# Performance work log

Measured on AMD Instinct MI355X. Metric: run time of the kernel, lower is better.

Reference implementation:

```python
import jax, jax.numpy as jnp
import numpy as np

V, E, H, L, B, S = 32000, 512, 512, 2, 8, 512


def setup_inputs() -> dict:
    key = jax.random.key(0)
    ks = jax.random.split(key, 16)
    emb = jax.random.normal(ks[0], (V, E), jnp.float32) * 0.02
    emb = emb.at[0].set(0.0)  # padding_idx=0
    init_state = jax.random.normal(ks[1], (2, L, H), jnp.float32)  # [h;c] params
    def xav(k, shp):
        fan_in, fan_out = shp[1], shp[0]
        lim = np.sqrt(6.0 / (fan_in + fan_out)).astype(np.float32)
        return jax.random.uniform(k, shp, jnp.float32, -lim, lim)
    inp = {
        'emb_table': emb,
        'init_state': init_state,
        'w_ih0': xav(ks[2], (4 * H, E)), 'w_hh0': xav(ks[3], (4 * H, H)),
        'b_ih0': jnp.zeros((4 * H,), jnp.float32), 'b_hh0': jnp.zeros((4 * H,), jnp.float32),
        'w_ih1': xav(ks[4], (4 * H, H)), 'w_hh1': xav(ks[5], (4 * H, H)),
        'b_ih1': jnp.zeros((4 * H,), jnp.float32), 'b_hh1': jnp.zeros((4 * H,), jnp.float32),
        'wg': xav(ks[6], (2 * H, H)), 'bg': jnp.zeros((2 * H,), jnp.float32),
        'wd': xav(ks[7], (V, H)), 'bd': jnp.zeros((V,), jnp.float32),
        'eps': jax.random.normal(ks[8], (B, S, H), jnp.float32),
        'x': jax.random.randint(ks[9], (B, S), 0, V, jnp.int64),
    }
    return inp


def _lstm_layer(xs, h0, c0, w_ih, w_hh, b_ih, b_hh):
    # xs: [S, B, in]; returns hidden sequence [S, B, H]
    b = b_ih + b_hh
    def step(carry, x_t):
        h, c = carry
        gates = x_t @ w_ih.T + h @ w_hh.T + b  # [B, 4H]
        i, f, g, o = jnp.split(gates, 4, axis=-1)  # torch gate order i,f,g,o
        c = jax.nn.sigmoid(f) * c + jax.nn.sigmoid(i) * jnp.tanh(g)
        h = jax.nn.sigmoid(o) * jnp.tanh(c)
        return (h, c), h
    _, hs = jax.lax.scan(step, (h0, c0), xs)
    return hs


def reference(emb_table, init_state, w_ih0, w_hh0, b_ih0, b_hh0,
              w_ih1, w_hh1, b_ih1, b_hh1, wg, bg, wd, bd, eps, x):
    Bsz = x.shape[0]
    embedding = emb_table[x]  # [B, S, E]
    h0 = jnp.broadcast_to(init_state[0][:, None, :], (L, Bsz, H))
    c0 = jnp.broadcast_to(init_state[1][:, None, :], (L, Bsz, H))
    xs = embedding.transpose(1, 0, 2)  # time-major [S, B, E]
    hs0 = _lstm_layer(xs, h0[0], c0[0], w_ih0, w_hh0, b_ih0, b_hh0)
    hs1 = _lstm_layer(hs0, h0[1], c0[1], w_ih1, w_hh1, b_ih1, b_hh1)
    out = hs1.transpose(1, 0, 2)  # [B, S, H]
    stats = out @ wg.T + bg  # [B, S, 2H]
    std = jax.nn.softplus(stats[:, :, :H])  # diagonal of covariance matrix
    mu = stats[:, :, H:]
    # MultivariateNormal(mu, cov=diag(std)).rsample() => mu + sqrt(std) * eps
    sample = mu + jnp.sqrt(std) * eps
    logits = sample @ wd.T + bd  # [B, S, V]
    return (logits, mu, std)
```

## Files before the change

kernel.cpp:

```cpp
#include <hip/hip_runtime.h>


typedef __attribute__((ext_vector_type(4))) float f32x4;
typedef __attribute__((ext_vector_type(8))) short short8;
typedef __attribute__((ext_vector_type(4))) unsigned short u16x4;

#define V_SZ 32000
#define E_SZ 512
#define H_SZ 512
#define B_SZ 8
#define S_SZ 512
#define NTOK 4096
#define G4H  2048

__device__ __forceinline__ unsigned short f2bf(float x) {
  unsigned int b = __float_as_uint(x);
  b += 0x7FFFu + ((b >> 16) & 1u);
  return (unsigned short)(b >> 16);
}
__device__ __forceinline__ float bf2f(unsigned short u) {
  return __uint_as_float(((unsigned int)u) << 16);
}

__device__ __forceinline__ void split4(const f32x4 v, u16x4& hv, u16x4& lv) {
  unsigned short h0 = f2bf(v.x); lv.x = f2bf(v.x - bf2f(h0)); hv.x = h0;
  unsigned short h1 = f2bf(v.y); lv.y = f2bf(v.y - bf2f(h1)); hv.y = h1;
  unsigned short h2 = f2bf(v.z); lv.z = f2bf(v.z - bf2f(h2)); hv.z = h2;
  unsigned short h3 = f2bf(v.w); lv.w = f2bf(v.w - bf2f(h3)); hv.w = h3;
}

__global__ void split_kernel(const float* __restrict__ src,
                             unsigned short* __restrict__ hi,
                             unsigned short* __restrict__ lo, int n4) {
  int i = blockIdx.x * 256 + threadIdx.x;
  if (i >= n4) return;
  f32x4 v = ((const f32x4*)src)[i];
  u16x4 hv, lv;
  split4(v, hv, lv);
  ((u16x4*)hi)[i] = hv;
  ((u16x4*)lo)[i] = lv;
}

__global__ void bias_sum_kernel(const float* __restrict__ a0, const float* __restrict__ c0,
                                const float* __restrict__ a1, const float* __restrict__ c1,
                                float* __restrict__ o0, float* __restrict__ o1) {
  int i = blockIdx.x * 256 + threadIdx.x;
  if (i < G4H) { o0[i] = a0[i] + c0[i]; o1[i] = a1[i] + c1[i]; }
}

__global__ void embed_hi_kernel(const float* __restrict__ emb, const int* __restrict__ x,
                                unsigned short* __restrict__ hi) {
  int gid = blockIdx.x * 256 + threadIdx.x;
  int r = gid >> 7;
  int kq = (gid & 127) << 2;
  int tok = x[r];
  f32x4 v = *(const f32x4*)(emb + (size_t)tok * E_SZ + kq);
  u16x4 hv;
  hv.x = f2bf(v.x); hv.y = f2bf(v.y); hv.z = f2bf(v.z); hv.w = f2bf(v.w);
  *(u16x4*)(hi + (size_t)r * E_SZ + kq) = hv;
}

__device__ __forceinline__ int swz32(int row, int seg) {
  return row * 32 + (((seg ^ (row & 3)) << 3));
}

__global__ __launch_bounds__(256, 2) void gemm2_kernel(
    const unsigned short* __restrict__ Ah,
    const unsigned short* __restrict__ Bh, const unsigned short* __restrict__ Bl,
    const float* __restrict__ bias, float* __restrict__ C,
    int M, int N, int K) {
  __shared__ unsigned short sA[128 * 32];
  __shared__ unsigned short sBh[128 * 32];
  __shared__ unsigned short sBl[128 * 32];

  const int t = threadIdx.x;
  const int lane = t & 63;
  const int wave = t >> 6;
  const int wr = wave >> 1, wc = wave & 1;
  const size_t m0 = (size_t)blockIdx.y * 128;
  const size_t n0 = (size_t)blockIdx.x * 128;

  f32x4 acc[4][4];
#pragma unroll
  for (int i = 0; i < 4; ++i)
#pragma unroll
    for (int j = 0; j < 4; ++j) acc[i][j] = (f32x4){0.f, 0.f, 0.f, 0.f};

  const int r0 = t >> 2;
  const int seg0 = t & 3;

  const int nk = K >> 5;
  for (int ks = 0; ks < nk; ++ks) {
    const int k0 = ks << 5;
    short8 vA[2], vBh[2], vBl[2];
#pragma unroll
    for (int r = 0; r < 2; ++r) {
      int row = r0 + r * 64;
      size_t ga = (m0 + row) * (size_t)K + k0 + seg0 * 8;
      size_t gb = (n0 + row) * (size_t)K + k0 + seg0 * 8;
      vA[r] = *(const short8*)(Ah + ga);
      vBh[r] = *(const short8*)(Bh + gb);
      vBl[r] = *(const short8*)(Bl + gb);
    }
    __syncthreads();
#pragma unroll
    for (int r = 0; r < 2; ++r) {
      int row = r0 + r * 64;
      int d = swz32(row, seg0);
      *(short8*)(sA + d) = vA[r];
      *(short8*)(sBh + d) = vBh[r];
      *(short8*)(sBl + d) = vBl[r];
    }
    __syncthreads();

    short8 a[4], bh[4], bl[4];
    const int seg = lane >> 4;
#pragma unroll
    for (int m = 0; m < 4; ++m) {
      int row = wr * 64 + m * 16 + (lane & 15);
      int d = swz32(row, seg);
      a[m] = *(const short8*)(sA + d);
    }
#pragma unroll
    for (int n = 0; n < 4; ++n) {
      int row = wc * 64 + n * 16 + (lane & 15);
      int d = swz32(row, seg);
      bh[n] = *(const short8*)(sBh + d);
      bl[n] = *(const short8*)(sBl + d);
    }
#pragma unroll
    for (int m = 0; m < 4; ++m) {
#pragma unroll
      for (int n = 0; n < 4; ++n) {
        acc[m][n] = __builtin_amdgcn_mfma_f32_16x16x32_bf16(a[m], bh[n], acc[m][n], 0, 0, 0);
        acc[m][n] = __builtin_amdgcn_mfma_f32_16x16x32_bf16(a[m], bl[n], acc[m][n], 0, 0, 0);
      }
    }
  }

#pragma unroll
  for (int m = 0; m < 4; ++m) {
#pragma unroll
    for (int n = 0; n < 4; ++n) {
      size_t gr0 = m0 + wr * 64 + m * 16 + ((lane >> 4) << 2);
      size_t gc = n0 + wc * 64 + n * 16 + (lane & 15);
      float bv = bias ? bias[gc] : 0.f;
#pragma unroll
      for (int j = 0; j < 4; ++j) {
        C[(gr0 + j) * (size_t)N + gc] = acc[m][n][j] + bv;
      }
    }
  }
}

#define SEQ_NB 192
#define SEQ_NB_L0 64

__device__ __forceinline__ float sigm(float x) { return 1.f / (1.f + expf(-x)); }

__global__ __launch_bounds__(256, 1) void lstm_seq_kernel(
    const float* __restrict__ gx0,
    const float* __restrict__ w_hh0,
    const float* __restrict__ w_ih1,
    const float* __restrict__ w_hh1,
    const float* __restrict__ b1s,
    const float* __restrict__ initst,
    float* __restrict__ h0_all,
    float* __restrict__ h1_all,
    unsigned short* __restrict__ hs1h,
    unsigned int* __restrict__ sig0,
    unsigned int* __restrict__ sig1) {
  const int blk = blockIdx.x;
  const int t = threadIdx.x;
  const bool isL1 = (blk >= SEQ_NB_L0);
  const int lb = isL1 ? (blk - SEQ_NB_L0) : blk;

  __shared__ float hA[8][512];
  __shared__ float hB[8][512];
  __shared__ float gates_s[32][8];

  const int tb = t >> 7;
  const int rg = isL1 ? ((t >> 5) & 3) : ((t >> 4) & 7);
  const int kg = isL1 ? (t & 31) : (t & 15);

  f32x4 w[4][8];
  if (!isL1) {
#pragma unroll
    for (int rr = 0; rr < 4; ++rr) {
      int rl = rg * 4 + rr;
      int grow = (rl >> 3) * H_SZ + lb * 8 + (rl & 7);
      const float* src = w_hh0 + (size_t)grow * H_SZ + kg * 4;
#pragma unroll
      for (int j = 0; j < 8; ++j) w[rr][j] = *(const f32x4*)(src + j * 64);
    }
  } else {
#pragma unroll
    for (int rr = 0; rr < 4; ++rr) {
      int rl = rg * 4 + rr;
      int grow = (rl >> 2) * H_SZ + lb * 4 + (rl & 3);
      const float* s1 = w_ih1 + (size_t)grow * H_SZ + kg * 4;
      const float* s2 = w_hh1 + (size_t)grow * H_SZ + kg * 4;
#pragma unroll
      for (int j = 0; j < 4; ++j) w[rr][j] = *(const f32x4*)(s1 + j * 128);
#pragma unroll
      for (int j = 0; j < 4; ++j) w[rr][4 + j] = *(const f32x4*)(s2 + j * 128);
    }
  }

  const int UPB = isL1 ? 4 : 8;
  const int nCell = UPB * 8;
  const int cu = t >> 3, cb = t & 7;
  const int cunit = lb * UPB + cu;
  float creg = 0.f;
  float bgi = 0.f, bgf = 0.f, bgg = 0.f, bgo = 0.f;
  if (t < nCell) {
    creg = initst[1024 + (isL1 ? 512 : 0) + cunit];
    if (isL1) {
      bgi = b1s[cunit];
      bgf = b1s[512 + cunit];
      bgg = b1s[1024 + cunit];
      bgo = b1s[1536 + cunit];
    }
  }

  for (int step = 0; step < 512; ++step) {
    float pgi = 0.f, pgf = 0.f, pgg = 0.f, pgo = 0.f;
    if (!isL1 && t < nCell) {
      const float* gx = gx0 + ((size_t)(cb * S_SZ + step)) * G4H + cunit;
      pgi = gx[0];
      pgf = gx[512];
      pgg = gx[1024];
      pgo = gx[1536];
    }

    if (t < 64) {
      if (!isL1) {
        if (step > 0) {
          const unsigned int* s0 = sig0 + (size_t)(step - 1) * 64;
          while (true) {
            unsigned int v = __hip_atomic_load(&s0[t], __ATOMIC_RELAXED, __HIP_MEMORY_SCOPE_AGENT);
            if (__all(v != 0)) break;
            __builtin_amdgcn_s_sleep(1);
          }
        }
      } else {
        const unsigned int* s0 = sig0 + (size_t)step * 64;
        const unsigned int* s1 = (step > 0) ? (sig1 + (size_t)(step - 1) * 128) : nullptr;
        while (true) {
          int ok = (__hip_atomic_load(&s0[t], __ATOMIC_RELAXED, __HIP_MEMORY_SCOPE_AGENT) != 0);
          if (s1) {
            ok &= (__hip_atomic_load(&s1[t], __ATOMIC_RELAXED, __HIP_MEMORY_SCOPE_AGENT) != 0);
            ok &= (__hip_atomic_load(&s1[64 + t], __ATOMIC_RELAXED, __HIP_MEMORY_SCOPE_AGENT) != 0);
          }
          if (__all(ok)) break;
          __builtin_amdgcn_s_sleep(1);
        }
      }
    }
    __syncthreads();

    if (!isL1) {
      if (step == 0) {
#pragma unroll
        for (int i = 0; i < 4; ++i) {
          int idx = t + i * 256;
          int b = idx >> 7;
          int kc = (idx & 127) << 2;
          *(f32x4*)&hA[b][kc] = *(const f32x4*)(initst + kc);
        }
      } else {
        const float* src = h0_all + (size_t)(step - 1) * 4096;
#pragma unroll
        for (int i = 0; i < 4; ++i) {
          int idx = t + i * 256;
          int b = idx >> 7;
          int kc = (idx & 127) << 2;
          *(f32x4*)&hA[b][kc] = *(const f32x4*)(src + b * H_SZ + kc);
        }
      }
    } else {
      const float* s0 = h0_all + (size_t)step * 4096;
      const float* s1 = (step == 0) ? nullptr : (h1_all + (size_t)(step - 1) * 4096);
#pragma unroll
      for (int i = 0; i < 4; ++i) {
        int idx = t + i * 256;
        int b = idx >> 7;
        int kc = (idx & 127) << 2;
        *(f32x4*)&hA[b][kc] = *(const f32x4*)(s0 + b * H_SZ + kc);
        f32x4 v1 = s1 ? *(const f32x4*)(s1 + b * H_SZ + kc)
                      : *(const f32x4*)(initst + 512 + kc);
        *(f32x4*)&hB[b][kc] = v1;
      }
    }
    __syncthreads();

    float acc[4][4];
#pragma unroll
    for (int rr = 0; rr < 4; ++rr)
#pragma unroll
      for (int bq = 0; bq < 4; ++bq) acc[rr][bq] = 0.f;

    if (!isL1) {
#pragma unroll
      for (int bq = 0; bq < 4; ++bq) {
        const float* hb = &hA[tb * 4 + bq][0];
#pragma unroll
        for (int j = 0; j < 8; ++j) {
          f32x4 hq = *(const f32x4*)(hb + kg * 4 + j * 64);
#pragma unroll
          for (int rr = 0; rr < 4; ++rr)
            acc[rr][bq] += w[rr][j].x * hq.x + w[rr][j].y * hq.y +
                           w[rr][j].z * hq.z + w[rr][j].w * hq.w;
        }
      }
#pragma unroll
      for (int s = 1; s < 16; s <<= 1) {
#pragma unroll
        for (int rr = 0; rr < 4; ++rr)
#pragma unroll
          for (int bq = 0; bq < 4; ++bq)
            acc[rr][bq] += __shfl_xor(acc[rr][bq], s, 64);
      }
      if (kg == 0) {
#pragma unroll
        for (int rr = 0; rr < 4; ++rr)
#pragma unroll
          for (int bq = 0; bq < 4; ++bq)
            gates_s[rg * 4 + rr][tb * 4 + bq] = acc[rr][bq];
      }
    } else {
#pragma unroll
      for (int bq = 0; bq < 4; ++bq) {
        const int b = tb * 4 + bq;
        const float* ha = &hA[b][0];
        const float* hbp = &hB[b][0];
#pragma unroll
        for (int j = 0; j < 4; ++j) {
          f32x4 hq = *(const f32x4*)(ha + kg * 4 + j * 128);
#pragma unroll
          for (int rr = 0; rr < 4; ++rr)
            acc[rr][bq] += w[rr][j].x * hq.x + w[rr][j].y * hq.y +
                           w[rr][j].z * hq.z + w[rr][j].w * hq.w;
        }
#pragma unroll
        for (int j = 0; j < 4; ++j) {
          f32x4 hq = *(const f32x4*)(hbp + kg * 4 + j * 128);
#pragma unroll
          for (int rr = 0; rr < 4; ++rr)
            acc[rr][bq] += w[rr][4 + j].x * hq.x + w[rr][4 + j].y * hq.y +
                           w[rr][4 + j].z * hq.z + w[rr][4 + j].w * hq.w;
        }
      }
#pragma unroll
      for (int s = 1; s < 32; s <<= 1) {
#pragma unroll
        for (int rr = 0; rr < 4; ++rr)
#pragma unroll
          for (int bq = 0; bq < 4; ++bq)
            acc[rr][bq] += __shfl_xor(acc[rr][bq], s, 64);
      }
      if (kg == 0) {
#pragma unroll
        for (int rr = 0; rr < 4; ++rr)
#pragma unroll
          for (int bq = 0; bq < 4; ++bq)
            gates_s[rg * 4 + rr][tb * 4 + bq] = acc[rr][bq];
      }
    }
    __syncthreads();

    float hval = 0.f;
    if (t < nCell) {
      float gi, gf, gg, go;
      if (!isL1) {
        gi = gates_s[cu][cb] + pgi;
        gf = gates_s[8 + cu][cb] + pgf;
        gg = gates_s[16 + cu][cb] + pgg;
        go = gates_s[24 + cu][cb] + pgo;
      } else {
        gi = gates_s[cu][cb] + bgi;
        gf = gates_s[4 + cu][cb] + bgf;
        gg = gates_s[8 + cu][cb] + bgg;
        go = gates_s[12 + cu][cb] + bgo;
      }
      float cn = sigm(gf) * creg + sigm(gi) * tanhf(gg);
      hval = sigm(go) * tanhf(cn);
      creg = cn;
      if (!isL1) {
        __hip_atomic_store(&h0_all[(size_t)step * 4096 + cb * H_SZ + cunit], hval,
                           __ATOMIC_RELAXED, __HIP_MEMORY_SCOPE_AGENT);
      } else {
        __hip_atomic_store(&h1_all[(size_t)step * 4096 + cb * H_SZ + cunit], hval,
                           __ATOMIC_RELAXED, __HIP_MEMORY_SCOPE_AGENT);
      }
    }
    if (t == 0) {
      asm volatile("s_waitcnt vmcnt(0)" ::: "memory");
      unsigned int* slot = isL1 ? (sig1 + (size_t)step * 128 + lb)
                                : (sig0 + (size_t)step * 64 + lb);
      __hip_atomic_store(slot, 1u, __ATOMIC_RELAXED, __HIP_MEMORY_SCOPE_AGENT);
    }
    if (isL1 && t < nCell) {
      hs1h[(size_t)(cb * S_SZ + step) * H_SZ + cunit] = f2bf(hval);
    }
  }
}

__global__ void sample_kernel(const float* __restrict__ stats, const float* __restrict__ eps,
                              unsigned short* __restrict__ sh,
                              float* __restrict__ omu, float* __restrict__ ostd) {
  int gid = blockIdx.x * 256 + threadIdx.x;
  int r = gid >> 9, hh = gid & 511;
  float sp = stats[(size_t)r * 1024 + hh];
  float mu = stats[(size_t)r * 1024 + 512 + hh];
  float sd = (sp > 20.f) ? sp : log1pf(expf(sp));
  float smp = mu + sqrtf(sd) * eps[gid];
  omu[gid] = mu;
  ostd[gid] = sd;
  sh[gid] = f2bf(smp);
}

extern "C" void kernel_launch(void* const* d_in, const int* in_sizes, int n_in,
                              void* d_out, int out_size, void* d_ws, size_t ws_size,
                              hipStream_t stream) {
  const float* emb    = (const float*)d_in[0];
  const float* initst = (const float*)d_in[1];
  const float* w_ih0  = (const float*)d_in[2];
  const float* w_hh0  = (const float*)d_in[3];
  const float* b_ih0  = (const float*)d_in[4];
  const float* b_hh0  = (const float*)d_in[5];
  const float* w_ih1  = (const float*)d_in[6];
  const float* w_hh1  = (const float*)d_in[7];
  const float* b_ih1  = (const float*)d_in[8];
  const float* b_hh1  = (const float*)d_in[9];
  const float* wg     = (const float*)d_in[10];
  const float* bg     = (const float*)d_in[11];
  const float* wd     = (const float*)d_in[12];
  const float* bd     = (const float*)d_in[13];
  const float* eps    = (const float*)d_in[14];
  const int*   x      = (const int*)d_in[15];

  char* ws = (char*)d_ws;
  size_t off = 0;
  auto alloc = [&](size_t sz) {
    void* p = ws + off;
    off = (off + sz + 255) & ~(size_t)255;
    return p;
  };
  unsigned int* sig0     = (unsigned int*)alloc((size_t)512 * 64 * 4);
  unsigned int* sig1     = (unsigned int*)alloc((size_t)512 * 128 * 4);
  float* b0s             = (float*)alloc(G4H * 4);
  float* b1s             = (float*)alloc(G4H * 4);
  unsigned short* wih0h  = (unsigned short*)alloc((size_t)G4H * E_SZ * 2);
  unsigned short* wih0l  = (unsigned short*)alloc((size_t)G4H * E_SZ * 2);
  unsigned short* wgh    = (unsigned short*)alloc((size_t)1024 * H_SZ * 2);
  unsigned short* wgl    = (unsigned short*)alloc((size_t)1024 * H_SZ * 2);
  unsigned short* wdh    = (unsigned short*)alloc((size_t)V_SZ * H_SZ * 2);
  unsigned short* wdl    = (unsigned short*)alloc((size_t)V_SZ * H_SZ * 2);
  unsigned short* a0h    = (unsigned short*)alloc((size_t)NTOK * E_SZ * 2);
  float* gx0             = (float*)alloc((size_t)NTOK * G4H * 4);
  float* h0_all          = (float*)alloc((size_t)512 * 4096 * 4);
  float* h1_all          = (float*)alloc((size_t)512 * 4096 * 4);
  unsigned short* hs1h   = (unsigned short*)alloc((size_t)NTOK * H_SZ * 2);
  float* stats           = (float*)alloc((size_t)NTOK * 1024 * 4);
  unsigned short* smph   = (unsigned short*)alloc((size_t)NTOK * H_SZ * 2);

  float* out_logits = (float*)d_out;
  float* out_mu     = out_logits + (size_t)NTOK * V_SZ;
  float* out_std    = out_mu + (size_t)NTOK * H_SZ;

  (void)hipMemsetAsync(sig0, 0, (size_t)512 * 64 * 4, stream);
  (void)hipMemsetAsync(sig1, 0, (size_t)512 * 128 * 4, stream);

  split_kernel<<<(G4H * E_SZ / 4 + 255) / 256, 256, 0, stream>>>(w_ih0, wih0h, wih0l, G4H * E_SZ / 4);
  split_kernel<<<(1024 * H_SZ / 4 + 255) / 256, 256, 0, stream>>>(wg, wgh, wgl, 1024 * H_SZ / 4);
  split_kernel<<<(V_SZ * H_SZ / 4 + 255) / 256, 256, 0, stream>>>(wd, wdh, wdl, V_SZ * H_SZ / 4);
  bias_sum_kernel<<<8, 256, 0, stream>>>(b_ih0, b_hh0, b_ih1, b_hh1, b0s, b1s);

  embed_hi_kernel<<<NTOK * 128 / 256, 256, 0, stream>>>(emb, x, a0h);

  gemm2_kernel<<<dim3(G4H / 128, NTOK / 128), 256, 0, stream>>>(
      a0h, wih0h, wih0l, b0s, gx0, NTOK, G4H, E_SZ);

  lstm_seq_kernel<<<SEQ_NB, 256, 0, stream>>>(
      gx0, w_hh0, w_ih1, w_hh1, b1s, initst, h0_all, h1_all, hs1h, sig0, sig1);

  gemm2_kernel<<<dim3(1024 / 128, NTOK / 128), 256, 0, stream>>>(
      hs1h, wgh, wgl, bg, stats, NTOK, 1024, H_SZ);

  sample_kernel<<<NTOK * H_SZ / 256, 256, 0, stream>>>(stats, eps, smph, out_mu, out_std);

  gemm2_kernel<<<dim3(V_SZ / 128, NTOK / 128), 256, 0, stream>>>(
      smph, wdh, wdl, bd, out_logits, NTOK, V_SZ, H_SZ);
}
```

Measured before the change: 3.693 ms.

## Use NaN-sentinel data polling for LSTM sync and single-bf16 decoder GEMM

The recurrent kernel drops its separate flag arrays. Consumers now poll the hidden-state buffers directly, which are pre-filled with an all-ones NaN sentinel, so each step needs one memory round trip instead of a flag check followed by a data load. Separately, the large vocabulary projection switches from a split hi/lo bf16 GEMM to a single bf16 GEMM with 2 blocks per CU. That halves MFMA work and weight traffic but reduces precision on the logits. The sentinel scheme assumes no real hidden value ever equals the 0xFFFFFFFF bit pattern, and that each 64-bit atomic load observes a consistent value.

```diff
diff --git a/kernel.cpp b/kernel.cpp
--- a/kernel.cpp
+++ b/kernel.cpp
@@ -27,6 +27,22 @@
   unsigned short h1 = f2bf(v.y); lv.y = f2bf(v.y - bf2f(h1)); hv.y = h1;
   unsigned short h2 = f2bf(v.z); lv.z = f2bf(v.z - bf2f(h2)); hv.z = h2;
   unsigned short h3 = f2bf(v.w); lv.w = f2bf(v.w - bf2f(h3)); hv.w = h3;
+}
+
+__device__ __forceinline__ f32x4 ld16_bypass(const float* p) {
+  const unsigned long long* q = (const unsigned long long*)p;
+  unsigned long long a = __hip_atomic_load(&q[0], __ATOMIC_RELAXED, __HIP_MEMORY_SCOPE_AGENT);
+  unsigned long long b = __hip_atomic_load(&q[1], __ATOMIC_RELAXED, __HIP_MEMORY_SCOPE_AGENT);
+  f32x4 r;
+  r.x = __uint_as_float((unsigned int)a);
+  r.y = __uint_as_float((unsigned int)(a >> 32));
+  r.z = __uint_as_float((unsigned int)b);
+  r.w = __uint_as_float((unsigned int)(b >> 32));
+  return r;
+}
+__device__ __forceinline__ int chk4(const f32x4 v) {
+  return (__float_as_uint(v.x) != 0xFFFFFFFFu) & (__float_as_uint(v.y) != 0xFFFFFFFFu) &
+         (__float_as_uint(v.z) != 0xFFFFFFFFu) & (__float_as_uint(v.w) != 0xFFFFFFFFu);
 }
 
 __global__ void split_kernel(const float* __restrict__ src,
@@ -41,6 +57,16 @@
   ((u16x4*)lo)[i] = lv;
 }
 
+__global__ void cast_hi_kernel(const float* __restrict__ src,
+                               unsigned short* __restrict__ hi, int n4) {
+  int i = blockIdx.x * 256 + threadIdx.x;
+  if (i >= n4) return;
+  f32x4 v = ((const f32x4*)src)[i];
+  u16x4 hv;
+  hv.x = f2bf(v.x); hv.y = f2bf(v.y); hv.z = f2bf(v.z); hv.w = f2bf(v.w);
+  ((u16x4*)hi)[i] = hv;
+}
+
 __global__ void bias_sum_kernel(const float* __restrict__ a0, const float* __restrict__ c0,
                                 const float* __restrict__ a1, const float* __restrict__ c1,
                                 float* __restrict__ o0, float* __restrict__ o1) {
@@ -118,8 +144,7 @@
 #pragma unroll
     for (int m = 0; m < 4; ++m) {
       int row = wr * 64 + m * 16 + (lane & 15);
-      int d = swz32(row, seg);
-      a[m] = *(const short8*)(sA + d);
+      a[m] = *(const short8*)(sA + swz32(row, seg));
     }
 #pragma unroll
     for (int n = 0; n < 4; ++n) {
@@ -134,6 +159,85 @@
       for (int n = 0; n < 4; ++n) {
         acc[m][n] = __builtin_amdgcn_mfma_f32_16x16x32_bf16(a[m], bh[n], acc[m][n], 0, 0, 0);
         acc[m][n] = __builtin_amdgcn_mfma_f32_16x16x32_bf16(a[m], bl[n], acc[m][n], 0, 0, 0);
+      }
+    }
+  }
+
+#pragma unroll
+  for (int m = 0; m < 4; ++m) {
+#pragma unroll
+    for (int n = 0; n < 4; ++n) {
+      size_t gr0 = m0 + wr * 64 + m * 16 + ((lane >> 4) << 2);
+      size_t gc = n0 + wc * 64 + n * 16 + (lane & 15);
+      float bv = bias ? bias[gc] : 0.f;
+#pragma unroll
+      for (int j = 0; j < 4; ++j) {
+        C[(gr0 + j) * (size_t)N + gc] = acc[m][n][j] + bv;
+      }
+    }
+  }
+}
+
+__global__ __launch_bounds__(256, 2) void gemm1_kernel(
+    const unsigned short* __restrict__ Ah, const unsigned short* __restrict__ Bh,
+    const float* __restrict__ bias, float* __restrict__ C,
+    int M, int N, int K) {
+  __shared__ unsigned short sA[128 * 32];
+  __shared__ unsigned short sB[128 * 32];
+
+  const int t = threadIdx.x;
+  const int lane = t & 63;
+  const int wave = t >> 6;
+  const int wr = wave >> 1, wc = wave & 1;
+  const size_t m0 = (size_t)blockIdx.y * 128;
+  const size_t n0 = (size_t)blockIdx.x * 128;
+
+  f32x4 acc[4][4];
+#pragma unroll
+  for (int i = 0; i < 4; ++i)
+#pragma unroll
+    for (int j = 0; j < 4; ++j) acc[i][j] = (f32x4){0.f, 0.f, 0.f, 0.f};
+
+  const int r0 = t >> 2;
+  const int seg0 = t & 3;
+
+  const int nk = K >> 5;
+  for (int ks = 0; ks < nk; ++ks) {
+    const int k0 = ks << 5;
+    short8 vA[2], vB[2];
+#pragma unroll
+    for (int r = 0; r < 2; ++r) {
+      int row = r0 + r * 64;
+      vA[r] = *(const short8*)(Ah + (m0 + row) * (size_t)K + k0 + seg0 * 8);
+      vB[r] = *(const short8*)(Bh + (n0 + row) * (size_t)K + k0 + seg0 * 8);
+    }
+    __syncthreads();
+#pragma unroll
+    for (int r = 0; r < 2; ++r) {
+      int row = r0 + r * 64;
+      int d = swz32(row, seg0);
+      *(short8*)(sA + d) = vA[r];
+      *(short8*)(sB + d) = vB[r];
+    }
+    __syncthreads();
+
+    short8 a[4], b[4];
+    const int seg = lane >> 4;
+#pragma unroll
+    for (int m = 0; m < 4; ++m) {
+      int row = wr * 64 + m * 16 + (lane & 15);
+      a[m] = *(const short8*)(sA + swz32(row, seg));
+    }
+#pragma unroll
+    for (int n = 0; n < 4; ++n) {
+      int row = wc * 64 + n * 16 + (lane & 15);
+      b[n] = *(const short8*)(sB + swz32(row, seg));
+    }
+#pragma unroll
+    for (int m = 0; m < 4; ++m) {
+#pragma unroll
+      for (int n = 0; n < 4; ++n) {
+        acc[m][n] = __builtin_amdgcn_mfma_f32_16x16x32_bf16(a[m], b[n], acc[m][n], 0, 0, 0);
       }
     }
   }
@@ -167,9 +271,7 @@
     const float* __restrict__ initst,
     float* __restrict__ h0_all,
     float* __restrict__ h1_all,
-    unsigned short* __restrict__ hs1h,
-    unsigned int* __restrict__ sig0,
-    unsigned int* __restrict__ sig1) {
+    unsigned short* __restrict__ hs1h) {
   const int blk = blockIdx.x;
   const int t = threadIdx.x;
   const bool isL1 = (blk >= SEQ_NB_L0);
@@ -233,63 +335,81 @@
       pgo = gx[1536];
     }
 
-    if (t < 64) {
-      if (!isL1) {
-        if (step > 0) {
-          const unsigned int* s0 = sig0 + (size_t)(step - 1) * 64;
-          while (true) {
-            unsigned int v = __hip_atomic_load(&s0[t], __ATOMIC_RELAXED, __HIP_MEMORY_SCOPE_AGENT);
-            if (__all(v != 0)) break;
-            __builtin_amdgcn_s_sleep(1);
-          }
+    float* ldA = &hA[0][0] + t * 4;
+    float* ldB = &hB[0][0] + t * 4;
+    if (!isL1) {
+      if (step == 0) {
+#pragma unroll
+        for (int i = 0; i < 4; ++i) {
+          int idx = t + i * 256;
+          int kc = (idx & 127) << 2;
+          *(f32x4*)(&hA[0][0] + idx * 4) = *(const f32x4*)(initst + kc);
         }
       } else {
-        const unsigned int* s0 = sig0 + (size_t)step * 64;
-        const unsigned int* s1 = (step > 0) ? (sig1 + (size_t)(step - 1) * 128) : nullptr;
+        const float* s = h0_all + (size_t)(step - 1) * 4096 + (size_t)t * 4;
+        f32x4 v0, v1, v2, v3;
         while (true) {
-          int ok = (__hip_atomic_load(&s0[t], __ATOMIC_RELAXED, __HIP_MEMORY_SCOPE_AGENT) != 0);
-          if (s1) {
-            ok &= (__hip_atomic_load(&s1[t], __ATOMIC_RELAXED, __HIP_MEMORY_SCOPE_AGENT) != 0);
-            ok &= (__hip_atomic_load(&s1[64 + t], __ATOMIC_RELAXED, __HIP_MEMORY_SCOPE_AGENT) != 0);
-          }
+          v0 = ld16_bypass(s);
+          v1 = ld16_bypass(s + 1024);
+          v2 = ld16_bypass(s + 2048);
+          v3 = ld16_bypass(s + 3072);
+          int ok = chk4(v0) & chk4(v1) & chk4(v2) & chk4(v3);
           if (__all(ok)) break;
           __builtin_amdgcn_s_sleep(1);
         }
-      }
-    }
-    __syncthreads();
-
-    if (!isL1) {
+        *(f32x4*)ldA = v0;
+        *(f32x4*)(ldA + 1024) = v1;
+        *(f32x4*)(ldA + 2048) = v2;
+        *(f32x4*)(ldA + 3072) = v3;
+      }
+    } else {
+      const float* s0 = h0_all + (size_t)step * 4096 + (size_t)t * 4;
       if (step == 0) {
+        f32x4 v0, v1, v2, v3;
+        while (true) {
+          v0 = ld16_bypass(s0);
+          v1 = ld16_bypass(s0 + 1024);
+          v2 = ld16_bypass(s0 + 2048);
+          v3 = ld16_bypass(s0 + 3072);
+          int ok = chk4(v0) & chk4(v1) & chk4(v2) & chk4(v3);
+          if (__all(ok)) break;
+          __builtin_amdgcn_s_sleep(1);
+        }
+        *(f32x4*)ldA = v0;
+        *(f32x4*)(ldA + 1024) = v1;
+        *(f32x4*)(ldA + 2048) = v2;
+        *(f32x4*)(ldA + 3072) = v3;
 #pragma unroll
         for (int i = 0; i < 4; ++i) {
           int idx = t + i * 256;
-          int b = idx >> 7;
           int kc = (idx & 127) << 2;
-          *(f32x4*)&hA[b][kc] = *(const f32x4*)(initst + kc);
+          *(f32x4*)(&hB[0][0] + idx * 4) = *(const f32x4*)(initst + 512 + kc);
         }
       } else {
-        const float* src = h0_all + (size_t)(step - 1) * 4096;
-#pragma unroll
-        for (int i = 0; i < 4; ++i) {
-          int idx = t + i * 256;
-          int b = idx >> 7;
-          int kc = (idx & 127) << 2;
-          *(f32x4*)&hA[b][kc] = *(const f32x4*)(src + b * H_SZ + kc);
-        }
-      }
-    } else {
-      const float* s0 = h0_all + (size_t)step * 4096;
-      const float* s1 = (step == 0) ? nullptr : (h1_all + (size_t)(step - 1) * 4096);
-#pragma unroll
-      for (int i = 0; i < 4; ++i) {
-        int idx = t + i * 256;
-        int b = idx >> 7;
-        int kc = (idx & 127) << 2;
-        *(f32x4*)&hA[b][kc] = *(const f32x4*)(s0 + b * H_SZ + kc);
-        f32x4 v1 = s1 ? *(const f32x4*)(s1 + b * H_SZ + kc)
-                      : *(const f32x4*)(initst + 512 + kc);
-        *(f32x4*)&hB[b][kc] = v1;
+        const float* s1 = h1_all + (size_t)(step - 1) * 4096 + (size_t)t * 4;
+        f32x4 a0, a1, a2, a3, b0, b1, b2, b3;
+        while (true) {
+          a0 = ld16_bypass(s0);
+          a1 = ld16_bypass(s0 + 1024);
+          a2 = ld16_bypass(s0 + 2048);
+          a3 = ld16_bypass(s0 + 3072);
+          b0 = ld16_bypass(s1);
+          b1 = ld16_bypass(s1 + 1024);
+          b2 = ld16_bypass(s1 + 2048);
+          b3 = ld16_bypass(s1 + 3072);
+          int ok = chk4(a0) & chk4(a1) & chk4(a2) & chk4(a3) &
+                   chk4(b0) & chk4(b1) & chk4(b2) & chk4(b3);
+          if (__all(ok)) break;
+          __builtin_amdgcn_s_sleep(1);
+        }
+        *(f32x4*)ldA = a0;
+        *(f32x4*)(ldA + 1024) = a1;
+        *(f32x4*)(ldA + 2048) = a2;
+        *(f32x4*)(ldA + 3072) = a3;
+        *(f32x4*)ldB = b0;
+        *(f32x4*)(ldB + 1024) = b1;
+        *(f32x4*)(ldB + 2048) = b2;
+        *(f32x4*)(ldB + 3072) = b3;
       }
     }
     __syncthreads();
@@ -369,7 +489,6 @@
     }
     __syncthreads();
 
-    float hval = 0.f;
     if (t < nCell) {
       float gi, gf, gg, go;
       if (!isL1) {
@@ -384,24 +503,14 @@
         go = gates_s[12 + cu][cb] + bgo;
       }
       float cn = sigm(gf) * creg + sigm(gi) * tanhf(gg);
-      hval = sigm(go) * tanhf(cn);
+      float hval = sigm(go) * tanhf(cn);
       creg = cn;
-      if (!isL1) {
-        __hip_atomic_store(&h0_all[(size_t)step * 4096 + cb * H_SZ + cunit], hval,
-                           __ATOMIC_RELAXED, __HIP_MEMORY_SCOPE_AGENT);
-      } else {
-        __hip_atomic_store(&h1_all[(size_t)step * 4096 + cb * H_SZ + cunit], hval,
-                           __ATOMIC_RELAXED, __HIP_MEMORY_SCOPE_AGENT);
-      }
-    }
-    if (t == 0) {
-      asm volatile("s_waitcnt vmcnt(0)" ::: "memory");
-      unsigned int* slot = isL1 ? (sig1 + (size_t)step * 128 + lb)
-                                : (sig0 + (size_t)step * 64 + lb);
-      __hip_atomic_store(slot, 1u, __ATOMIC_RELAXED, __HIP_MEMORY_SCOPE_AGENT);
-    }
-    if (isL1 && t < nCell) {
-      hs1h[(size_t)(cb * S_SZ + step) * H_SZ + cunit] = f2bf(hval);
+      float* hbase = isL1 ? h1_all : h0_all;
+      __hip_atomic_store(&hbase[(size_t)step * 4096 + cb * H_SZ + cunit], hval,
+                         __ATOMIC_RELAXED, __HIP_MEMORY_SCOPE_AGENT);
+      if (isL1) {
+        hs1h[(size_t)(cb * S_SZ + step) * H_SZ + cunit] = f2bf(hval);
+      }
     }
   }
 }
@@ -447,8 +556,6 @@
     off = (off + sz + 255) & ~(size_t)255;
     return p;
   };
-  unsigned int* sig0     = (unsigned int*)alloc((size_t)512 * 64 * 4);
-  unsigned int* sig1     = (unsigned int*)alloc((size_t)512 * 128 * 4);
   float* b0s             = (float*)alloc(G4H * 4);
   float* b1s             = (float*)alloc(G4H * 4);
   unsigned short* wih0h  = (unsigned short*)alloc((size_t)G4H * E_SZ * 2);
@@ -456,7 +563,6 @@
   unsigned short* wgh    = (unsigned short*)alloc((size_t)1024 * H_SZ * 2);
   unsigned short* wgl    = (unsigned short*)alloc((size_t)1024 * H_SZ * 2);
   unsigned short* wdh    = (unsigned short*)alloc((size_t)V_SZ * H_SZ * 2);
-  unsigned short* wdl    = (unsigned short*)alloc((size_t)V_SZ * H_SZ * 2);
   unsigned short* a0h    = (unsigned short*)alloc((size_t)NTOK * E_SZ * 2);
   float* gx0             = (float*)alloc((size_t)NTOK * G4H * 4);
   float* h0_all          = (float*)alloc((size_t)512 * 4096 * 4);
@@ -469,12 +575,12 @@
   float* out_mu     = out_logits + (size_t)NTOK * V_SZ;
   float* out_std    = out_mu + (size_t)NTOK * H_SZ;
 
-  (void)hipMemsetAsync(sig0, 0, (size_t)512 * 64 * 4, stream);
-  (void)hipMemsetAsync(sig1, 0, (size_t)512 * 128 * 4, stream);
+  (void)hipMemsetAsync(h0_all, 0xFF, (size_t)512 * 4096 * 4, stream);
+  (void)hipMemsetAsync(h1_all, 0xFF, (size_t)512 * 4096 * 4, stream);
 
   split_kernel<<<(G4H * E_SZ / 4 + 255) / 256, 256, 0, stream>>>(w_ih0, wih0h, wih0l, G4H * E_SZ / 4);
   split_kernel<<<(1024 * H_SZ / 4 + 255) / 256, 256, 0, stream>>>(wg, wgh, wgl, 1024 * H_SZ / 4);
-  split_kernel<<<(V_SZ * H_SZ / 4 + 255) / 256, 256, 0, stream>>>(wd, wdh, wdl, V_SZ * H_SZ / 4);
+  cast_hi_kernel<<<(V_SZ * H_SZ / 4 + 255) / 256, 256, 0, stream>>>(wd, wdh, V_SZ * H_SZ / 4);
   bias_sum_kernel<<<8, 256, 0, stream>>>(b_ih0, b_hh0, b_ih1, b_hh1, b0s, b1s);
 
   embed_hi_kernel<<<NTOK * 128 / 256, 256, 0, stream>>>(emb, x, a0h);
@@ -483,13 +589,13 @@
       a0h, wih0h, wih0l, b0s, gx0, NTOK, G4H, E_SZ);
 
   lstm_seq_kernel<<<SEQ_NB, 256, 0, stream>>>(
-      gx0, w_hh0, w_ih1, w_hh1, b1s, initst, h0_all, h1_all, hs1h, sig0, sig1);
+      gx0, w_hh0, w_ih1, w_hh1, b1s, initst, h0_all, h1_all, hs1h);
 
   gemm2_kernel<<<dim3(1024 / 128, NTOK / 128), 256, 0, stream>>>(
       hs1h, wgh, wgl, bg, stats, NTOK, 1024, H_SZ);
 
   sample_kernel<<<NTOK * H_SZ / 256, 256, 0, stream>>>(stats, eps, smph, out_mu, out_std);
 
-  gemm2_kernel<<<dim3(V_SZ / 128, NTOK / 128), 256, 0, stream>>>(
-      smph, wdh, wdl, bd, out_logits, NTOK, V_SZ, H_SZ);
-}
+  gemm1_kernel<<<dim3(V_SZ / 128, NTOK / 128), 256, 0, stream>>>(
+      smph, wdh, bd, out_logits, NTOK, V_SZ, H_SZ);
+}
```

Result: slower. 4.142 ms (+12.2%).
